# Performance work log

Hardware: AMD Instinct MI355X
Metric: run time of the kernel (lower is better)

Reference implementation:

```python
import jax, jax.numpy as jnp
import numpy as np

BATCH_SIZE = 512
N_PARTS = 4
TEMP_FAC = 0.1
D = 4096
EPS = 1e-6


def _static_indices():
    # bs and factor per the n_parts==4, batch_size!=12 branch
    bs = 4 * BATCH_SIZE
    factor = 10 * N_PARTS
    pos = np.arange(bs)
    active = pos[pos % (3 * N_PARTS) < N_PARTS]            # positions that contribute
    # i1..i6 = (pos + k*n_parts) % bs for k = 0..5
    I = (active[:, None] + np.arange(6)[None, :] * N_PARTS) % bs   # (P, 6)
    # denominator indices removed: (pos + k*n_parts) % bs for k = 0..factor*n_parts-1
    offs = (active[:, None] + np.arange(factor * N_PARTS)[None, :] * N_PARTS) % bs
    M = np.ones((active.shape[0], bs), dtype=np.float32)
    M[np.arange(active.shape[0])[:, None], offs] = 0.0     # (P, bs) denominator mask
    return I, M

_I, _M = _static_indices()
# symmetrical-loss pairs: (i1,i2),(i2,i3),(i1,i4),(i4,i5),(i5,i6),(i2,i5),(i3,i6)
_PAIRS = [(0, 1), (1, 2), (0, 3), (3, 4), (4, 5), (1, 4), (2, 5)]


def setup_inputs() -> dict:
    key = jax.random.key(0)
    reg_pred = jax.random.normal(key, (4 * BATCH_SIZE, D), dtype=jnp.float32)
    return {"reg_pred": reg_pred}


def reference(reg_pred):
    I = jnp.asarray(_I)
    M = jnp.asarray(_M)
    norms = jnp.linalg.norm(reg_pred, axis=1)              # (bs,)
    # torch CosineSimilarity: dot / max(||a||*||b||, eps)
    gram = reg_pred @ reg_pred.T                           # (bs, bs)
    S = gram / jnp.maximum(norms[:, None] * norms[None, :], EPS) / TEMP_FAC
    E = jnp.exp(S)                                         # (bs, bs)
    # denominator exp-sums for each anchor role k at each active position p
    Dsum = jnp.einsum('pkb,pb->pk', E[I], M)               # (P, 6)
    total = jnp.float32(0.0)
    for a, b in _PAIRS:
        num = S[I[:, a], I[:, b]]                          # (P,)
        en = jnp.exp(num)
        total = total + jnp.sum(-jnp.log(en / (en + Dsum[:, a]))
                                - jnp.log(en / (en + Dsum[:, b])))
    return total / (6 * BATCH_SIZE)
```

## Files before the change

### kernel.cpp

```cpp
#include <hip/hip_runtime.h>
#include <hip/hip_bf16.h>
#include <stdint.h>

#define NROWS 2048
#define DIM   4096
#define NACT  684
#define INV_TEMP 10.0f
#define NTILE 136
#define KSPLIT 4
#define KSEG  1024
#define KITER 32
#define FP8_SCALE 16.0f
#define PART_SCALE (1.0f / 256.0f)

#define WAITCNT_VM0   0x0F70
#define WAITCNT_VM2   0x0F72
#define WAITCNT_VM4   0x0F74
#define WAITCNT_VM6   0x0F76

typedef __attribute__((ext_vector_type(4))) float floatx4;
typedef __attribute__((ext_vector_type(8))) short shortx8;
typedef __attribute__((ext_vector_type(8))) unsigned short ushortx8;

static __device__ __forceinline__ unsigned short f32_to_bf16(float f) {
  union { float f; unsigned int u; } v; v.f = f;
  unsigned int u = v.u;
  unsigned int r = u + 0x7fffu + ((u >> 16) & 1u);
  return (unsigned short)(r >> 16);
}
static __device__ __forceinline__ float bf16_to_f32(unsigned short u) {
  union { unsigned int u; float f; } v; v.u = ((unsigned int)u) << 16;
  return v.f;
}
static __device__ __forceinline__ unsigned short f32_to_f16(float f) {
  _Float16 h = (_Float16)f;
  union { _Float16 h; unsigned short u; } v; v.h = h;
  return v.u;
}
static __device__ __forceinline__ float f16_to_f32(unsigned short u) {
  union { unsigned short u; _Float16 h; } v; v.u = u;
  return (float)v.h;
}

__global__ __launch_bounds__(256) void k_normconv_fp8(const float* __restrict__ X,
                                                      unsigned char* __restrict__ Yq) {
  const int row = blockIdx.x;
  const float4* xr = (const float4*)(X + (size_t)row * DIM);
  float4 v[4];
  float s = 0.f;
#pragma unroll
  for (int t = 0; t < 4; t++) {
    float4 w = xr[threadIdx.x * 4 + t];
    v[t] = w;
    s += w.x * w.x + w.y * w.y + w.z * w.z + w.w * w.w;
  }
#pragma unroll
  for (int off = 32; off > 0; off >>= 1) s += __shfl_down(s, off, 64);
  __shared__ float wsum[4];
  if ((threadIdx.x & 63) == 0) wsum[threadIdx.x >> 6] = s;
  __syncthreads();
  const float total = wsum[0] + wsum[1] + wsum[2] + wsum[3];
  const float sc = FP8_SCALE / fmaxf(sqrtf(total), 1e-30f);
  uint4 o;
  unsigned int r0;
  r0 = __builtin_amdgcn_cvt_pk_fp8_f32(v[0].x * sc, v[0].y * sc, 0, false);
  o.x = __builtin_amdgcn_cvt_pk_fp8_f32(v[0].z * sc, v[0].w * sc, r0, true);
  r0 = __builtin_amdgcn_cvt_pk_fp8_f32(v[1].x * sc, v[1].y * sc, 0, false);
  o.y = __builtin_amdgcn_cvt_pk_fp8_f32(v[1].z * sc, v[1].w * sc, r0, true);
  r0 = __builtin_amdgcn_cvt_pk_fp8_f32(v[2].x * sc, v[2].y * sc, 0, false);
  o.z = __builtin_amdgcn_cvt_pk_fp8_f32(v[2].z * sc, v[2].w * sc, r0, true);
  r0 = __builtin_amdgcn_cvt_pk_fp8_f32(v[3].x * sc, v[3].y * sc, 0, false);
  o.w = __builtin_amdgcn_cvt_pk_fp8_f32(v[3].z * sc, v[3].w * sc, r0, true);
  ((uint4*)(Yq + (size_t)row * DIM))[threadIdx.x] = o;
}

__global__ __launch_bounds__(256) void k_gemm_sym(const unsigned char* __restrict__ Yq,
                                                  unsigned short* __restrict__ P) {
  __shared__ __attribute__((aligned(16))) unsigned char lds[4 * 8192];
  const int bid = blockIdx.x;
  const int kz = bid & 3;
  const int t  = bid >> 2;
  int ti = 0, rem = t;
  while (rem >= 16 - ti) { rem -= 16 - ti; ti++; }
  const int tj = ti + rem;
  const int row0 = ti * 128;
  const int col0 = tj * 128;
  const int kbase = kz * KSEG;

  const int tid  = threadIdx.x;
  const int lane = tid & 63;
  const int wave = tid >> 6;
  const int wr = wave >> 1;
  const int wc = wave & 1;

  floatx4 zero = {0.f, 0.f, 0.f, 0.f};
  floatx4 acc[4][4];
#pragma unroll
  for (int i = 0; i < 4; i++)
#pragma unroll
    for (int j = 0; j < 4; j++) acc[i][j] = zero;

  const unsigned char* gA = Yq + (size_t)(row0 + (tid >> 1)) * DIM + kbase + (tid & 1) * 16;
  const unsigned char* gB = Yq + (size_t)(col0 + (tid >> 1)) * DIM + kbase + (tid & 1) * 16;

  const int fr  = lane & 15;
  const int fc8 = (lane >> 4) * 8;

#define ISSUE(st, koff)                                                                \
  do {                                                                                 \
    __builtin_amdgcn_global_load_lds(                                                  \
        (const __attribute__((address_space(1))) void*)(gA + (koff)),                  \
        (__attribute__((address_space(3))) void*)(lds + (st) * 8192 + tid * 16),       \
        16, 0, 0);                                                                     \
    __builtin_amdgcn_global_load_lds(                                                  \
        (const __attribute__((address_space(1))) void*)(gB + (koff)),                  \
        (__attribute__((address_space(3))) void*)(lds + (st) * 8192 + 4096 + tid * 16),\
        16, 0, 0);                                                                     \
  } while (0)

#define COMPUTE(st)                                                                    \
  do {                                                                                 \
    const unsigned char* bA = lds + (st) * 8192;                                       \
    const unsigned char* bB = bA + 4096;                                               \
    long long af[4], bf[4];                                                            \
    _Pragma("unroll")                                                                  \
    for (int mi = 0; mi < 4; mi++)                                                     \
      af[mi] = *(const long long*)(bA + (wr * 64 + mi * 16 + fr) * 32 + fc8);          \
    _Pragma("unroll")                                                                  \
    for (int ni = 0; ni < 4; ni++)                                                     \
      bf[ni] = *(const long long*)(bB + (wc * 64 + ni * 16 + fr) * 32 + fc8);          \
    _Pragma("unroll")                                                                  \
    for (int mi = 0; mi < 4; mi++)                                                     \
      _Pragma("unroll")                                                                \
      for (int ni = 0; ni < 4; ni++)                                                   \
        acc[mi][ni] = __builtin_amdgcn_mfma_f32_16x16x32_fp8_fp8(af[mi], bf[ni],       \
                                                                 acc[mi][ni], 0, 0, 0);\
  } while (0)

  ISSUE(0, 0);
  ISSUE(1, 32);
  ISSUE(2, 64);
#pragma unroll 4
  for (int k = 0; k < KITER; k++) {
    const int cur = k & 3;
    if (k < KITER - 3) {
      ISSUE((k + 3) & 3, (k + 3) * 32);
      __builtin_amdgcn_s_waitcnt(WAITCNT_VM6);
    } else if (k == KITER - 3) {
      __builtin_amdgcn_s_waitcnt(WAITCNT_VM4);
    } else if (k == KITER - 2) {
      __builtin_amdgcn_s_waitcnt(WAITCNT_VM2);
    } else {
      __builtin_amdgcn_s_waitcnt(WAITCNT_VM0);
    }
    __builtin_amdgcn_sched_barrier(0);
    __builtin_amdgcn_s_barrier();
    COMPUTE(cur);
    if (k < KITER - 1) {
      __builtin_amdgcn_s_barrier();
      __builtin_amdgcn_sched_barrier(0);
    }
  }

#undef ISSUE
#undef COMPUTE

  unsigned short* dst = P + (size_t)(t * KSPLIT + kz) * 16384;
  const int cc  = lane & 15;
  const int cr4 = (lane >> 4) * 4;
#pragma unroll
  for (int mi = 0; mi < 4; mi++) {
    const int row = wr * 64 + mi * 16 + cr4;
#pragma unroll
    for (int ni = 0; ni < 4; ni++) {
      const int col = wc * 64 + ni * 16 + cc;
      unsigned int d0 = (unsigned int)f32_to_bf16(acc[mi][ni][0] * PART_SCALE) |
                        ((unsigned int)f32_to_bf16(acc[mi][ni][1] * PART_SCALE) << 16);
      unsigned int d1 = (unsigned int)f32_to_bf16(acc[mi][ni][2] * PART_SCALE) |
                        ((unsigned int)f32_to_bf16(acc[mi][ni][3] * PART_SCALE) << 16);
      uint2 v; v.x = d0; v.y = d1;
      *(uint2*)(dst + (size_t)col * 128 + row) = v;
    }
  }
}

__global__ __launch_bounds__(256) void k_combine(const unsigned short* __restrict__ P,
                                                 unsigned short* __restrict__ S,
                                                 float* __restrict__ T) {
  __shared__ float tileS[32][132];
  __shared__ float tileE[32][132];
  const int t = blockIdx.x;
  const int h = blockIdx.y;
  int ti = 0, rem = t;
  while (rem >= 16 - ti) { rem -= 16 - ti; ti++; }
  const int tj = ti + rem;
  const int gr = ti * 128, gc = tj * 128;
  const int c0 = h * 32;
  const int tid = threadIdx.x;
  const int cl = tid >> 3;
  const int q  = tid & 7;

  float acc[16];
#pragma unroll
  for (int j = 0; j < 16; j++) acc[j] = 0.f;
#pragma unroll
  for (int kz = 0; kz < KSPLIT; kz++) {
    const ushortx8* p = (const ushortx8*)(P + (size_t)(t * KSPLIT + kz) * 16384 +
                                          (size_t)(c0 + cl) * 128 + q * 16);
#pragma unroll
    for (int c = 0; c < 2; c++) {
      ushortx8 u = p[c];
#pragma unroll
      for (int e = 0; e < 8; e++) acc[c * 8 + e] += bf16_to_f32((unsigned short)u[e]);
    }
  }
  float cs = 0.f;
  unsigned short hv[16];
#pragma unroll
  for (int j = 0; j < 16; j++) {
    float v = acc[j] * INV_TEMP;
    float ev = __expf(v);
    hv[j] = f32_to_f16(v);
    tileS[cl][q * 16 + j] = v;
    tileE[cl][q * 16 + j] = ev;
    cs += ev;
  }
  {
    uint4* srow = (uint4*)(S + (size_t)(gc + c0 + cl) * NROWS + gr + q * 16);
#pragma unroll
    for (int u = 0; u < 2; u++) {
      uint4 w;
      w.x = (unsigned int)hv[u * 8 + 0] | ((unsigned int)hv[u * 8 + 1] << 16);
      w.y = (unsigned int)hv[u * 8 + 2] | ((unsigned int)hv[u * 8 + 3] << 16);
      w.z = (unsigned int)hv[u * 8 + 4] | ((unsigned int)hv[u * 8 + 5] << 16);
      w.w = (unsigned int)hv[u * 8 + 6] | ((unsigned int)hv[u * 8 + 7] << 16);
      srow[u] = w;
    }
  }
  cs += __shfl_xor(cs, 1, 64);
  cs += __shfl_xor(cs, 2, 64);
  cs += __shfl_xor(cs, 4, 64);
  if (q == 0) atomicAdd(&T[gc + c0 + cl], cs);

  if (ti != tj) {
    __syncthreads();
    const int r = tid >> 1;
    const int hh = tid & 1;
    float rs = 0.f;
    unsigned short hv2[16];
#pragma unroll
    for (int e = 0; e < 16; e++) {
      hv2[e] = f32_to_f16(tileS[hh * 16 + e][r]);
      rs += tileE[hh * 16 + e][r];
    }
    uint4* drow = (uint4*)(S + (size_t)(gr + r) * NROWS + gc + c0 + hh * 16);
#pragma unroll
    for (int u = 0; u < 2; u++) {
      uint4 w;
      w.x = (unsigned int)hv2[u * 8 + 0] | ((unsigned int)hv2[u * 8 + 1] << 16);
      w.y = (unsigned int)hv2[u * 8 + 2] | ((unsigned int)hv2[u * 8 + 3] << 16);
      w.z = (unsigned int)hv2[u * 8 + 4] | ((unsigned int)hv2[u * 8 + 5] << 16);
      w.w = (unsigned int)hv2[u * 8 + 6] | ((unsigned int)hv2[u * 8 + 7] << 16);
      drow[u] = w;
    }
    rs += __shfl_xor(rs, 1, 64);
    if (hh == 0) atomicAdd(&T[gr + r], rs);
  }
}

__global__ __launch_bounds__(64) void k_dsum_h(const unsigned short* __restrict__ S,
                                               const float* __restrict__ T,
                                               float* __restrict__ Ds) {
  const int p = blockIdx.x;
  const int k = blockIdx.y;
  const int a = 12 * (p >> 2) + (p & 3);
  const int lane = threadIdx.x;
  const int row = (a + 4 * k) & (NROWS - 1);
  const int m = a >> 2;
  const int c = a & 3;
  const uint2* sr = (const uint2*)(S + (size_t)row * NROWS);
  float s = 0.f;
  {
    uint2 v0 = sr[(m + lane) & 511];
    uint2 v1 = sr[(m + 64 + lane) & 511];
    unsigned short e0 = (c < 2) ? (unsigned short)(v0.x >> (16 * c))
                                : (unsigned short)(v0.y >> (16 * (c - 2)));
    unsigned short e1 = (c < 2) ? (unsigned short)(v1.x >> (16 * c))
                                : (unsigned short)(v1.y >> (16 * (c - 2)));
    s += __expf(f16_to_f32(e0)) + __expf(f16_to_f32(e1));
    if (lane < 32) {
      uint2 v2 = sr[(m + 128 + lane) & 511];
      unsigned short e2 = (c < 2) ? (unsigned short)(v2.x >> (16 * c))
                                  : (unsigned short)(v2.y >> (16 * (c - 2)));
      s += __expf(f16_to_f32(e2));
    }
  }
#pragma unroll
  for (int off = 32; off > 0; off >>= 1) s += __shfl_down(s, off, 64);
  if (lane == 0) Ds[p * 6 + k] = T[row] - s;
}

__global__ __launch_bounds__(256) void k_final_h(const unsigned short* __restrict__ S,
                                                 const float* __restrict__ Ds,
                                                 float* __restrict__ out) {
  const int pa[7] = {0, 1, 0, 3, 4, 1, 2};
  const int pb[7] = {1, 2, 3, 4, 5, 4, 5};
  const int idx = blockIdx.x * 256 + threadIdx.x;
  float s = 0.f;
  if (idx < NACT * 7) {
    const int p = idx / 7;
    const int q = idx - p * 7;
    const int a0 = 12 * (p >> 2) + (p & 3);
    const int ra = (a0 + 4 * pa[q]) & (NROWS - 1);
    const int rb = (a0 + 4 * pb[q]) & (NROWS - 1);
    const float num = f16_to_f32(S[(size_t)ra * NROWS + rb]);
    const float en = __expf(num);
    s = __logf(en + Ds[p * 6 + pa[q]]) + __logf(en + Ds[p * 6 + pb[q]]) - 2.f * num;
  }
#pragma unroll
  for (int off = 32; off > 0; off >>= 1) s += __shfl_down(s, off, 64);
  if ((threadIdx.x & 63) == 0) atomicAdd(out, s * (1.0f / (6.0f * 512.0f)));
}

__global__ __launch_bounds__(256) void k_normconv(const float* __restrict__ X,
                                                  unsigned short* __restrict__ Y) {
  const int row = blockIdx.x;
  const float4* xr = (const float4*)(X + (size_t)row * DIM);
  float4 v[4];
  float s = 0.f;
#pragma unroll
  for (int t = 0; t < 4; t++) {
    float4 w = xr[threadIdx.x + t * 256];
    v[t] = w;
    s += w.x * w.x + w.y * w.y + w.z * w.z + w.w * w.w;
  }
#pragma unroll
  for (int off = 32; off > 0; off >>= 1) s += __shfl_down(s, off, 64);
  __shared__ float wsum[4];
  if ((threadIdx.x & 63) == 0) wsum[threadIdx.x >> 6] = s;
  __syncthreads();
  const float total = wsum[0] + wsum[1] + wsum[2] + wsum[3];
  const float inv = 1.0f / fmaxf(sqrtf(total), 1e-30f);
  ushort4* yr = (ushort4*)(Y + (size_t)row * DIM);
#pragma unroll
  for (int t = 0; t < 4; t++) {
    float4 w = v[t];
    ushort4 o;
    o.x = f32_to_bf16(w.x * inv);
    o.y = f32_to_bf16(w.y * inv);
    o.z = f32_to_bf16(w.z * inv);
    o.w = f32_to_bf16(w.w * inv);
    yr[threadIdx.x + t * 256] = o;
  }
}

__global__ __launch_bounds__(256) void k_gemm(const unsigned short* __restrict__ Y,
                                              float* __restrict__ S) {
  __shared__ __attribute__((aligned(16))) unsigned short sA[128 * 32];
  __shared__ __attribute__((aligned(16))) unsigned short sB[128 * 32];
  const int tid  = threadIdx.x;
  const int lane = tid & 63;
  const int wave = tid >> 6;
  const int wr = wave >> 1;
  const int wc = wave & 1;
  const int row0 = blockIdx.y * 128;
  const int col0 = blockIdx.x * 128;

  floatx4 zero = {0.f, 0.f, 0.f, 0.f};
  floatx4 acc[4][4];
#pragma unroll
  for (int i = 0; i < 4; i++)
#pragma unroll
    for (int j = 0; j < 4; j++) acc[i][j] = zero;

  const int sr = tid >> 2;
  const int sc = (tid & 3) * 8;
  const unsigned short* gA0 = Y + (size_t)(row0 + sr) * DIM + sc;
  const unsigned short* gA1 = gA0 + (size_t)64 * DIM;
  const unsigned short* gB0 = Y + (size_t)(col0 + sr) * DIM + sc;
  const unsigned short* gB1 = gB0 + (size_t)64 * DIM;

  const int fr = lane & 15;
  const int fc = (lane >> 4) * 8;

  for (int k0 = 0; k0 < DIM; k0 += 32) {
    __builtin_amdgcn_global_load_lds(
        (const __attribute__((address_space(1))) void*)(gA0 + k0),
        (__attribute__((address_space(3))) void*)(sA + tid * 8), 16, 0, 0);
    __builtin_amdgcn_global_load_lds(
        (const __attribute__((address_space(1))) void*)(gA1 + k0),
        (__attribute__((address_space(3))) void*)(sA + 2048 + tid * 8), 16, 0, 0);
    __builtin_amdgcn_global_load_lds(
        (const __attribute__((address_space(1))) void*)(gB0 + k0),
        (__attribute__((address_space(3))) void*)(sB + tid * 8), 16, 0, 0);
    __builtin_amdgcn_global_load_lds(
        (const __attribute__((address_space(1))) void*)(gB1 + k0),
        (__attribute__((address_space(3))) void*)(sB + 2048 + tid * 8), 16, 0, 0);
    __syncthreads();

    shortx8 af[4], bf[4];
#pragma unroll
    for (int mi = 0; mi < 4; mi++)
      af[mi] = *(const shortx8*)(sA + (wr * 64 + mi * 16 + fr) * 32 + fc);
#pragma unroll
    for (int ni = 0; ni < 4; ni++)
      bf[ni] = *(const shortx8*)(sB + (wc * 64 + ni * 16 + fr) * 32 + fc);
#pragma unroll
    for (int mi = 0; mi < 4; mi++)
#pragma unroll
      for (int ni = 0; ni < 4; ni++)
        acc[mi][ni] = __builtin_amdgcn_mfma_f32_16x16x32_bf16(af[mi], bf[ni], acc[mi][ni], 0, 0, 0);
    __syncthreads();
  }

  const int cc  = lane & 15;
  const int cr4 = (lane >> 4) * 4;
#pragma unroll
  for (int mi = 0; mi < 4; mi++) {
    const int row = row0 + wr * 64 + mi * 16 + cr4;
#pragma unroll
    for (int ni = 0; ni < 4; ni++) {
      const int col = col0 + wc * 64 + ni * 16 + cc;
      float* dst = S + (size_t)row * NROWS + col;
#pragma unroll
      for (int r = 0; r < 4; r++) dst[(size_t)r * NROWS] = acc[mi][ni][r] * INV_TEMP;
    }
  }
}

__global__ __launch_bounds__(256) void k_rowsum(const float* __restrict__ S,
                                                float* __restrict__ T) {
  const int row = blockIdx.x;
  const float* sr = S + (size_t)row * NROWS;
  float s = 0.f;
  for (int b = threadIdx.x; b < NROWS; b += 256) s += __expf(sr[b]);
#pragma unroll
  for (int off = 32; off > 0; off >>= 1) s += __shfl_down(s, off, 64);
  __shared__ float wsum[4];
  if ((threadIdx.x & 63) == 0) wsum[threadIdx.x >> 6] = s;
  __syncthreads();
  if (threadIdx.x == 0) T[row] = wsum[0] + wsum[1] + wsum[2] + wsum[3];
}

__global__ __launch_bounds__(64) void k_dsum(const float* __restrict__ S,
                                             const float* __restrict__ T,
                                             float* __restrict__ Ds) {
  const int p = blockIdx.x;
  const int k = blockIdx.y;
  const int a = 12 * (p >> 2) + (p & 3);
  const int lane = threadIdx.x;
  const int row = (a + 4 * k) & (NROWS - 1);
  const int m = a >> 2;
  const int c = a & 3;
  const float4* sr4 = (const float4*)(S + (size_t)row * NROWS);
  float s = 0.f;
  {
    float4 v0 = sr4[(m + lane) & 511];
    float4 v1 = sr4[(m + 64 + lane) & 511];
    float e0 = c == 0 ? v0.x : c == 1 ? v0.y : c == 2 ? v0.z : v0.w;
    float e1 = c == 0 ? v1.x : c == 1 ? v1.y : c == 2 ? v1.z : v1.w;
    s += __expf(e0) + __expf(e1);
    if (lane < 32) {
      float4 v2 = sr4[(m + 128 + lane) & 511];
      float e2 = c == 0 ? v2.x : c == 1 ? v2.y : c == 2 ? v2.z : v2.w;
      s += __expf(e2);
    }
  }
#pragma unroll
  for (int off = 32; off > 0; off >>= 1) s += __shfl_down(s, off, 64);
  if (lane == 0) Ds[p * 6 + k] = T[row] - s;
}

__global__ __launch_bounds__(256) void k_final(const float* __restrict__ S,
                                               const float* __restrict__ Ds,
                                               float* __restrict__ out) {
  const int pa[7] = {0, 1, 0, 3, 4, 1, 2};
  const int pb[7] = {1, 2, 3, 4, 5, 4, 5};
  const int idx = blockIdx.x * 256 + threadIdx.x;
  float s = 0.f;
  if (idx < NACT * 7) {
    const int p = idx / 7;
    const int q = idx - p * 7;
    const int a0 = 12 * (p >> 2) + (p & 3);
    const int ra = (a0 + 4 * pa[q]) & (NROWS - 1);
    const int rb = (a0 + 4 * pb[q]) & (NROWS - 1);
    const float num = S[(size_t)ra * NROWS + rb];
    const float en = __expf(num);
    s = __logf(en + Ds[p * 6 + pa[q]]) + __logf(en + Ds[p * 6 + pb[q]]) - 2.f * num;
  }
#pragma unroll
  for (int off = 32; off > 0; off >>= 1) s += __shfl_down(s, off, 64);
  if ((threadIdx.x & 63) == 0) atomicAdd(out, s * (1.0f / (6.0f * 512.0f)));
}

extern "C" void kernel_launch(void* const* d_in, const int* in_sizes, int n_in,
                              void* d_out, int out_size, void* d_ws, size_t ws_size,
                              hipStream_t stream) {
  const float* X = (const float*)d_in[0];
  char* ws = (char*)d_ws;
  float* out = (float*)d_out;

  const size_t pOff = (size_t)32 * 1024 * 1024;
  const size_t pBytes = (size_t)NTILE * KSPLIT * 16384 * 2;
  const size_t needA = pOff + pBytes + 8192 + NACT * 6 * 4 + 256;

  hipMemsetAsync(out, 0, sizeof(float), stream);

  if (ws_size >= needA) {
    unsigned char* Yq = (unsigned char*)ws;
    unsigned short* S16 = (unsigned short*)(ws + (size_t)16 * 1024 * 1024);
    unsigned short* P = (unsigned short*)(ws + pOff);
    float* T  = (float*)(ws + pOff + pBytes);
    float* Ds = (float*)(ws + pOff + pBytes + 8192);
    hipMemsetAsync(T, 0, NROWS * sizeof(float), stream);
    hipLaunchKernelGGL(k_normconv_fp8, dim3(NROWS), dim3(256), 0, stream, X, Yq);
    hipLaunchKernelGGL(k_gemm_sym, dim3(NTILE * KSPLIT), dim3(256), 0, stream, Yq, P);
    hipLaunchKernelGGL(k_combine, dim3(NTILE, 4), dim3(256), 0, stream, P, S16, T);
    hipLaunchKernelGGL(k_dsum_h, dim3(NACT, 6), dim3(64), 0, stream, S16, T, Ds);
    hipLaunchKernelGGL(k_final_h, dim3((NACT * 7 + 255) / 256), dim3(256), 0, stream, S16, Ds, out);
  } else {
    unsigned short* Y = (unsigned short*)ws;
    float* S = (float*)(ws + (size_t)16 * 1024 * 1024);
    float* T  = (float*)(ws + pOff);
    float* Ds = (float*)(ws + pOff + 8192);
    hipLaunchKernelGGL(k_normconv, dim3(NROWS), dim3(256), 0, stream, X, Y);
    hipLaunchKernelGGL(k_gemm, dim3(16, 16), dim3(256), 0, stream, Y, S);
    hipLaunchKernelGGL(k_rowsum, dim3(NROWS), dim3(256), 0, stream, S, T);
    hipLaunchKernelGGL(k_dsum, dim3(NACT, 6), dim3(64), 0, stream, S, T, Ds);
    hipLaunchKernelGGL(k_final, dim3((NACT * 7 + 255) / 256), dim3(256), 0, stream, S, Ds, out);
  }
}
```

Baseline: 121.8 us.

## Switch FP8 GEMM to 32x32x64 scaled MFMA and fuse tail kernels

```diff
diff --git a/kernel.cpp b/kernel.cpp
--- a/kernel.cpp
+++ b/kernel.cpp
@@ -9,16 +9,19 @@
 #define NTILE 136
 #define KSPLIT 4
 #define KSEG  1024
-#define KITER 32
+#define KIT   16
 #define FP8_SCALE 16.0f
 #define PART_SCALE (1.0f / 256.0f)
 
 #define WAITCNT_VM0   0x0F70
-#define WAITCNT_VM2   0x0F72
 #define WAITCNT_VM4   0x0F74
-#define WAITCNT_VM6   0x0F76
+#define WAITCNT_VM8   0x0F78
+#define WAITCNT_VM12  0x0F7C
 
 typedef __attribute__((ext_vector_type(4))) float floatx4;
+typedef __attribute__((ext_vector_type(16))) float floatx16;
+typedef __attribute__((ext_vector_type(4))) int intx4;
+typedef __attribute__((ext_vector_type(8))) int intx8;
 typedef __attribute__((ext_vector_type(8))) short shortx8;
 typedef __attribute__((ext_vector_type(8))) unsigned short ushortx8;
 
@@ -43,8 +46,12 @@
 }
 
 __global__ __launch_bounds__(256) void k_normconv_fp8(const float* __restrict__ X,
-                                                      unsigned char* __restrict__ Yq) {
+                                                      unsigned char* __restrict__ Yq,
+                                                      float* __restrict__ T,
+                                                      float* __restrict__ out) {
   const int row = blockIdx.x;
+  if (threadIdx.x == 0) T[row] = 0.f;
+  if (row == 0 && threadIdx.x == 64) *out = 0.f;
   const float4* xr = (const float4*)(X + (size_t)row * DIM);
   float4 v[4];
   float s = 0.f;
@@ -74,9 +81,9 @@
   ((uint4*)(Yq + (size_t)row * DIM))[threadIdx.x] = o;
 }
 
-__global__ __launch_bounds__(256) void k_gemm_sym(const unsigned char* __restrict__ Yq,
-                                                  unsigned short* __restrict__ P) {
-  __shared__ __attribute__((aligned(16))) unsigned char lds[4 * 8192];
+__global__ __launch_bounds__(256) void k_gemm_mx(const unsigned char* __restrict__ Yq,
+                                                 unsigned short* __restrict__ P) {
+  __shared__ __attribute__((aligned(16))) unsigned char lds[4 * 16384];
   const int bid = blockIdx.x;
   const int kz = bid & 3;
   const int t  = bid >> 2;
@@ -93,70 +100,99 @@
   const int wr = wave >> 1;
   const int wc = wave & 1;
 
-  floatx4 zero = {0.f, 0.f, 0.f, 0.f};
-  floatx4 acc[4][4];
-#pragma unroll
-  for (int i = 0; i < 4; i++)
-#pragma unroll
-    for (int j = 0; j < 4; j++) acc[i][j] = zero;
-
-  const unsigned char* gA = Yq + (size_t)(row0 + (tid >> 1)) * DIM + kbase + (tid & 1) * 16;
-  const unsigned char* gB = Yq + (size_t)(col0 + (tid >> 1)) * DIM + kbase + (tid & 1) * 16;
-
-  const int fr  = lane & 15;
-  const int fc8 = (lane >> 4) * 8;
-
-#define ISSUE(st, koff)                                                                \
-  do {                                                                                 \
-    __builtin_amdgcn_global_load_lds(                                                  \
-        (const __attribute__((address_space(1))) void*)(gA + (koff)),                  \
-        (__attribute__((address_space(3))) void*)(lds + (st) * 8192 + tid * 16),       \
-        16, 0, 0);                                                                     \
-    __builtin_amdgcn_global_load_lds(                                                  \
-        (const __attribute__((address_space(1))) void*)(gB + (koff)),                  \
-        (__attribute__((address_space(3))) void*)(lds + (st) * 8192 + 4096 + tid * 16),\
-        16, 0, 0);                                                                     \
+  floatx16 zero = {0.f, 0.f, 0.f, 0.f, 0.f, 0.f, 0.f, 0.f,
+                   0.f, 0.f, 0.f, 0.f, 0.f, 0.f, 0.f, 0.f};
+  floatx16 acc[2][2];
+#pragma unroll
+  for (int i = 0; i < 2; i++)
+#pragma unroll
+    for (int j = 0; j < 2; j++) acc[i][j] = zero;
+
+  const int r2  = tid >> 2;
+  const int c16 = tid & 3;
+  const unsigned int swst = (unsigned)(((r2 >> 1) & 3) << 4);
+  const unsigned int colst = ((unsigned)(c16 << 4)) ^ swst;
+  const unsigned char* gA = Yq + (size_t)(row0 + r2) * DIM + kbase + colst;
+  const unsigned char* gB = Yq + (size_t)(col0 + r2) * DIM + kbase + colst;
+
+#define ISSUE(st, koff)                                                                  \
+  do {                                                                                   \
+    __builtin_amdgcn_global_load_lds(                                                    \
+        (const __attribute__((address_space(1))) void*)(gA + (koff)),                    \
+        (__attribute__((address_space(3))) void*)(lds + (st) * 16384 + tid * 16),        \
+        16, 0, 0);                                                                       \
+    __builtin_amdgcn_global_load_lds(                                                    \
+        (const __attribute__((address_space(1))) void*)(gA + (size_t)64 * DIM + (koff)), \
+        (__attribute__((address_space(3))) void*)(lds + (st) * 16384 + 4096 + tid * 16), \
+        16, 0, 0);                                                                       \
+    __builtin_amdgcn_global_load_lds(                                                    \
+        (const __attribute__((address_space(1))) void*)(gB + (koff)),                    \
+        (__attribute__((address_space(3))) void*)(lds + (st) * 16384 + 8192 + tid * 16), \
+        16, 0, 0);                                                                       \
+    __builtin_amdgcn_global_load_lds(                                                    \
+        (const __attribute__((address_space(1))) void*)(gB + (size_t)64 * DIM + (koff)), \
+        (__attribute__((address_space(3))) void*)(lds + (st) * 16384 + 12288 + tid * 16),\
+        16, 0, 0);                                                                       \
   } while (0)
 
-#define COMPUTE(st)                                                                    \
-  do {                                                                                 \
-    const unsigned char* bA = lds + (st) * 8192;                                       \
-    const unsigned char* bB = bA + 4096;                                               \
-    long long af[4], bf[4];                                                            \
-    _Pragma("unroll")                                                                  \
-    for (int mi = 0; mi < 4; mi++)                                                     \
-      af[mi] = *(const long long*)(bA + (wr * 64 + mi * 16 + fr) * 32 + fc8);          \
-    _Pragma("unroll")                                                                  \
-    for (int ni = 0; ni < 4; ni++)                                                     \
-      bf[ni] = *(const long long*)(bB + (wc * 64 + ni * 16 + fr) * 32 + fc8);          \
-    _Pragma("unroll")                                                                  \
-    for (int mi = 0; mi < 4; mi++)                                                     \
-      _Pragma("unroll")                                                                \
-      for (int ni = 0; ni < 4; ni++)                                                   \
-        acc[mi][ni] = __builtin_amdgcn_mfma_f32_16x16x32_fp8_fp8(af[mi], bf[ni],       \
-                                                                 acc[mi][ni], 0, 0, 0);\
+#define COMPUTE(st)                                                                      \
+  do {                                                                                   \
+    const unsigned char* bA = lds + (st) * 16384;                                        \
+    const unsigned char* bB = bA + 8192;                                                 \
+    const unsigned int c0 = (unsigned)((lane >> 5) << 5);                                \
+    intx8 af[2], bf[2];                                                                  \
+    _Pragma("unroll")                                                                    \
+    for (int mi = 0; mi < 2; mi++) {                                                     \
+      const int r = wr * 64 + mi * 32 + (lane & 31);                                     \
+      const unsigned int sw = (unsigned)(((r >> 1) & 3) << 4);                           \
+      const unsigned char* base = bA + r * 64;                                           \
+      intx4 lo = *(const intx4*)(base + (c0 ^ sw));                                      \
+      intx4 hi = *(const intx4*)(base + ((c0 ^ sw) ^ 16u));                              \
+      intx8 v;                                                                           \
+      v[0] = lo[0]; v[1] = lo[1]; v[2] = lo[2]; v[3] = lo[3];                            \
+      v[4] = hi[0]; v[5] = hi[1]; v[6] = hi[2]; v[7] = hi[3];                            \
+      af[mi] = v;                                                                        \
+    }                                                                                    \
+    _Pragma("unroll")                                                                    \
+    for (int ni = 0; ni < 2; ni++) {                                                     \
+      const int r = wc * 64 + ni * 32 + (lane & 31);                                     \
+      const unsigned int sw = (unsigned)(((r >> 1) & 3) << 4);                           \
+      const unsigned char* base = bB + r * 64;                                           \
+      intx4 lo = *(const intx4*)(base + (c0 ^ sw));                                      \
+      intx4 hi = *(const intx4*)(base + ((c0 ^ sw) ^ 16u));                              \
+      intx8 v;                                                                           \
+      v[0] = lo[0]; v[1] = lo[1]; v[2] = lo[2]; v[3] = lo[3];                            \
+      v[4] = hi[0]; v[5] = hi[1]; v[6] = hi[2]; v[7] = hi[3];                            \
+      bf[ni] = v;                                                                        \
+    }                                                                                    \
+    _Pragma("unroll")                                                                    \
+    for (int mi = 0; mi < 2; mi++)                                                       \
+      _Pragma("unroll")                                                                  \
+      for (int ni = 0; ni < 2; ni++)                                                     \
+        acc[mi][ni] = __builtin_amdgcn_mfma_scale_f32_32x32x64_f8f6f4(                   \
+            af[mi], bf[ni], acc[mi][ni], 0, 0, 0, 0x7F7F7F7F, 0, 0x7F7F7F7F);            \
   } while (0)
 
   ISSUE(0, 0);
-  ISSUE(1, 32);
-  ISSUE(2, 64);
+  ISSUE(1, 64);
+  ISSUE(2, 128);
 #pragma unroll 4
-  for (int k = 0; k < KITER; k++) {
+  for (int k = 0; k < KIT; k++) {
     const int cur = k & 3;
-    if (k < KITER - 3) {
-      ISSUE((k + 3) & 3, (k + 3) * 32);
-      __builtin_amdgcn_s_waitcnt(WAITCNT_VM6);
-    } else if (k == KITER - 3) {
+    if (k < KIT - 3) {
+      ISSUE((k + 3) & 3, (k + 3) * 64);
+      __builtin_amdgcn_s_waitcnt(WAITCNT_VM12);
+    } else if (k == KIT - 3) {
+      __builtin_amdgcn_s_waitcnt(WAITCNT_VM8);
+    } else if (k == KIT - 2) {
       __builtin_amdgcn_s_waitcnt(WAITCNT_VM4);
-    } else if (k == KITER - 2) {
-      __builtin_amdgcn_s_waitcnt(WAITCNT_VM2);
     } else {
       __builtin_amdgcn_s_waitcnt(WAITCNT_VM0);
     }
     __builtin_amdgcn_sched_barrier(0);
     __builtin_amdgcn_s_barrier();
     COMPUTE(cur);
-    if (k < KITER - 1) {
+    if (k < KIT - 1) {
       __builtin_amdgcn_s_barrier();
       __builtin_amdgcn_sched_barrier(0);
     }
@@ -166,20 +202,23 @@
 #undef COMPUTE
 
   unsigned short* dst = P + (size_t)(t * KSPLIT + kz) * 16384;
-  const int cc  = lane & 15;
-  const int cr4 = (lane >> 4) * 4;
-#pragma unroll
-  for (int mi = 0; mi < 4; mi++) {
-    const int row = wr * 64 + mi * 16 + cr4;
-#pragma unroll
-    for (int ni = 0; ni < 4; ni++) {
-      const int col = wc * 64 + ni * 16 + cc;
-      unsigned int d0 = (unsigned int)f32_to_bf16(acc[mi][ni][0] * PART_SCALE) |
-                        ((unsigned int)f32_to_bf16(acc[mi][ni][1] * PART_SCALE) << 16);
-      unsigned int d1 = (unsigned int)f32_to_bf16(acc[mi][ni][2] * PART_SCALE) |
-                        ((unsigned int)f32_to_bf16(acc[mi][ni][3] * PART_SCALE) << 16);
-      uint2 v; v.x = d0; v.y = d1;
-      *(uint2*)(dst + (size_t)col * 128 + row) = v;
+  const int cc = lane & 31;
+  const int cr = (lane >> 5) * 4;
+#pragma unroll
+  for (int mi = 0; mi < 2; mi++) {
+#pragma unroll
+    for (int ni = 0; ni < 2; ni++) {
+      const int col = wc * 64 + ni * 32 + cc;
+#pragma unroll
+      for (int q = 0; q < 4; q++) {
+        const int row = wr * 64 + mi * 32 + q * 8 + cr;
+        unsigned int d0 = (unsigned int)f32_to_bf16(acc[mi][ni][q * 4 + 0] * PART_SCALE) |
+                          ((unsigned int)f32_to_bf16(acc[mi][ni][q * 4 + 1] * PART_SCALE) << 16);
+        unsigned int d1 = (unsigned int)f32_to_bf16(acc[mi][ni][q * 4 + 2] * PART_SCALE) |
+                          ((unsigned int)f32_to_bf16(acc[mi][ni][q * 4 + 3] * PART_SCALE) << 16);
+        uint2 v; v.x = d0; v.y = d1;
+        *(uint2*)(dst + (size_t)col * 128 + row) = v;
+      }
     }
   }
 }
@@ -268,13 +307,15 @@
   }
 }
 
-__global__ __launch_bounds__(64) void k_dsum_h(const unsigned short* __restrict__ S,
-                                               const float* __restrict__ T,
-                                               float* __restrict__ Ds) {
+__global__ __launch_bounds__(384) void k_tail(const unsigned short* __restrict__ S,
+                                              const float* __restrict__ T,
+                                              float* __restrict__ out) {
+  __shared__ float ds_s[6];
   const int p = blockIdx.x;
-  const int k = blockIdx.y;
   const int a = 12 * (p >> 2) + (p & 3);
-  const int lane = threadIdx.x;
+  const int tid = threadIdx.x;
+  const int k = tid >> 6;
+  const int lane = tid & 63;
   const int row = (a + 4 * k) & (NROWS - 1);
   const int m = a >> 2;
   const int c = a & 3;
@@ -297,29 +338,25 @@
   }
 #pragma unroll
   for (int off = 32; off > 0; off >>= 1) s += __shfl_down(s, off, 64);
-  if (lane == 0) Ds[p * 6 + k] = T[row] - s;
-}
-
-__global__ __launch_bounds__(256) void k_final_h(const unsigned short* __restrict__ S,
-                                                 const float* __restrict__ Ds,
-                                                 float* __restrict__ out) {
-  const int pa[7] = {0, 1, 0, 3, 4, 1, 2};
-  const int pb[7] = {1, 2, 3, 4, 5, 4, 5};
-  const int idx = blockIdx.x * 256 + threadIdx.x;
-  float s = 0.f;
-  if (idx < NACT * 7) {
-    const int p = idx / 7;
-    const int q = idx - p * 7;
-    const int a0 = 12 * (p >> 2) + (p & 3);
-    const int ra = (a0 + 4 * pa[q]) & (NROWS - 1);
-    const int rb = (a0 + 4 * pb[q]) & (NROWS - 1);
+  if (lane == 0) ds_s[k] = T[row] - s;
+  __syncthreads();
+
+  float r = 0.f;
+  if (tid < 7) {
+    const int pa[7] = {0, 1, 0, 3, 4, 1, 2};
+    const int pb[7] = {1, 2, 3, 4, 5, 4, 5};
+    const int ra = (a + 4 * pa[tid]) & (NROWS - 1);
+    const int rb = (a + 4 * pb[tid]) & (NROWS - 1);
     const float num = f16_to_f32(S[(size_t)ra * NROWS + rb]);
     const float en = __expf(num);
-    s = __logf(en + Ds[p * 6 + pa[q]]) + __logf(en + Ds[p * 6 + pb[q]]) - 2.f * num;
-  }
-#pragma unroll
-  for (int off = 32; off > 0; off >>= 1) s += __shfl_down(s, off, 64);
-  if ((threadIdx.x & 63) == 0) atomicAdd(out, s * (1.0f / (6.0f * 512.0f)));
+    r = __logf(en + ds_s[pa[tid]]) + __logf(en + ds_s[pb[tid]]) - 2.f * num;
+  }
+  if (tid < 64) {
+    r += __shfl_down(r, 4, 64);
+    r += __shfl_down(r, 2, 64);
+    r += __shfl_down(r, 1, 64);
+    if (tid == 0) atomicAdd(out, r * (1.0f / (6.0f * 512.0f)));
+  }
 }
 
 __global__ __launch_bounds__(256) void k_normconv(const float* __restrict__ X,
@@ -504,25 +541,21 @@
   const size_t pBytes = (size_t)NTILE * KSPLIT * 16384 * 2;
   const size_t needA = pOff + pBytes + 8192 + NACT * 6 * 4 + 256;
 
-  hipMemsetAsync(out, 0, sizeof(float), stream);
-
   if (ws_size >= needA) {
     unsigned char* Yq = (unsigned char*)ws;
     unsigned short* S16 = (unsigned short*)(ws + (size_t)16 * 1024 * 1024);
     unsigned short* P = (unsigned short*)(ws + pOff);
     float* T  = (float*)(ws + pOff + pBytes);
-    float* Ds = (float*)(ws + pOff + pBytes + 8192);
-    hipMemsetAsync(T, 0, NROWS * sizeof(float), stream);
-    hipLaunchKernelGGL(k_normconv_fp8, dim3(NROWS), dim3(256), 0, stream, X, Yq);
-    hipLaunchKernelGGL(k_gemm_sym, dim3(NTILE * KSPLIT), dim3(256), 0, stream, Yq, P);
+    hipLaunchKernelGGL(k_normconv_fp8, dim3(NROWS), dim3(256), 0, stream, X, Yq, T, out);
+    hipLaunchKernelGGL(k_gemm_mx, dim3(NTILE * KSPLIT), dim3(256), 0, stream, Yq, P);
     hipLaunchKernelGGL(k_combine, dim3(NTILE, 4), dim3(256), 0, stream, P, S16, T);
-    hipLaunchKernelGGL(k_dsum_h, dim3(NACT, 6), dim3(64), 0, stream, S16, T, Ds);
-    hipLaunchKernelGGL(k_final_h, dim3((NACT * 7 + 255) / 256), dim3(256), 0, stream, S16, Ds, out);
+    hipLaunchKernelGGL(k_tail, dim3(NACT), dim3(384), 0, stream, S16, T, out);
   } else {
     unsigned short* Y = (unsigned short*)ws;
     float* S = (float*)(ws + (size_t)16 * 1024 * 1024);
     float* T  = (float*)(ws + pOff);
     float* Ds = (float*)(ws + pOff + 8192);
+    hipMemsetAsync(out, 0, sizeof(float), stream);
     hipLaunchKernelGGL(k_normconv, dim3(NROWS), dim3(256), 0, stream, X, Y);
     hipLaunchKernelGGL(k_gemm, dim3(16, 16), dim3(256), 0, stream, Y, S);
     hipLaunchKernelGGL(k_rowsum, dim3(NROWS), dim3(256), 0, stream, S, T);
```

New measurement: 110.8 us. 9.0% less time.
